# Optimization experiments

Measured on AMD Instinct MI355X. Metric: run time of the kernel, lower is better.

Reference implementation:

```python
import jax, jax.numpy as jnp
import numpy as np

NUM_CLASSES = 80
ANCHORS = np.array([[10,13],[16,30],[33,23],[30,61],[62,45],[59,119],[116,90],[156,198],[373,326]], np.float32)
MASK = [[0,1,2],[3,4,5],[6,7,8]]
STRIDES = [8, 16, 32]
MAX_OUT = 100      # max_output_size_per_class == max_total_size
IOU_THR = 0.45
SCORE_THR = 0.25
NMS_TOPK = 128     # per-class candidate pre-selection for greedy NMS (>= MAX_OUT)


def setup_inputs() -> dict:
    key = jax.random.key(0)
    k1, k2, k3 = jax.random.split(key, 3)
    B = 16
    C = 3 * (NUM_CLASSES + 5)  # 255
    return {
        'p3': jax.random.normal(k1, (B, 80, 80, C), jnp.float32),
        'p4': jax.random.normal(k2, (B, 40, 40, C), jnp.float32),
        'p5': jax.random.normal(k3, (B, 20, 20, C), jnp.float32),
    }


def _decode(logits, anchors, stride):
    # logits: [B,H,W,3*(nc+5)] -> boxes [B,H*W*3,4] (x1y1x2y2), obj [B,M], cls [B,M,nc]
    B, H, W, _ = logits.shape
    A = anchors.shape[0]
    x = logits.reshape(B, H, W, A, NUM_CLASSES + 5)
    xy = jax.nn.sigmoid(x[..., :2])
    wh_logit = x[..., 2:4]
    obj = jax.nn.sigmoid(x[..., 4])
    cls = jax.nn.sigmoid(x[..., 5:])
    gx, gy = jnp.meshgrid(jnp.arange(W, dtype=x.dtype), jnp.arange(H, dtype=x.dtype))
    grid = jnp.stack([gx, gy], axis=-1)[:, :, None, :]  # [H,W,1,2]
    ctr = (xy + grid) * stride
    wh = jnp.exp(wh_logit) * anchors  # [B,H,W,A,2]
    box = jnp.concatenate([ctr - wh / 2.0, ctr + wh / 2.0], axis=-1)
    return box.reshape(B, -1, 4), obj.reshape(B, -1), cls.reshape(B, -1, NUM_CLASSES)


def _pairwise_iou(b):
    # b: [K,4] x1y1x2y2 -> [K,K]
    area = (b[:, 2] - b[:, 0]) * (b[:, 3] - b[:, 1])
    lt = jnp.maximum(b[:, None, :2], b[None, :, :2])
    rb = jnp.minimum(b[:, None, 2:], b[None, :, 2:])
    wh = jnp.clip(rb - lt, 0.0)
    inter = wh[..., 0] * wh[..., 1]
    return inter / (area[:, None] + area[None, :] - inter + 1e-9)


def _nms_single(boxes, scores):
    # boxes [N,4], scores [N] for one (image, class): greedy NMS on top-K candidates
    s = jnp.where(scores > SCORE_THR, scores, -1.0)
    top_s, idx = jax.lax.top_k(s, NMS_TOPK)   # sorted descending
    b = boxes[idx]                            # [K,4]
    iou = _pairwise_iou(b)                    # [K,K]
    rng = jnp.arange(NMS_TOPK)

    def body(keep, i):
        active = keep[i] & (top_s[i] > 0.0)
        sup = active & (iou[i] > IOU_THR) & (rng > i)
        return keep & ~sup, None

    keep, _ = jax.lax.scan(body, jnp.ones(NMS_TOPK, bool), rng)
    valid = keep & (top_s > 0.0)
    ss = jnp.where(valid, top_s, -1.0)
    sel_s, sel_i = jax.lax.top_k(ss, MAX_OUT)
    return b[sel_i], sel_s                    # [M,4], [M]


def _per_image(boxes, scores_cn):
    # boxes [N,4] shared across classes (q=1), scores_cn [C,N]
    cb, cs = jax.vmap(_nms_single, in_axes=(None, 0))(boxes, scores_cn)  # [C,M,4],[C,M]
    C = cs.shape[0]
    cls_id = jnp.broadcast_to(jnp.arange(C, dtype=boxes.dtype)[:, None], cs.shape)
    fs, fi = jax.lax.top_k(cs.reshape(-1), MAX_OUT)
    fb = cb.reshape(-1, 4)[fi]
    fc = cls_id.reshape(-1)[fi]
    valid = fs > 0.0
    n_valid = jnp.sum(valid).astype(jnp.int32)
    return (jnp.where(valid[:, None], fb, 0.0),
            jnp.where(valid, fs, 0.0),
            jnp.where(valid, fc, 0.0),
            n_valid)


def _forward(p3, p4, p5):
    boxes, objs, clss = [], [], []
    for logits, m, stride in zip((p3, p4, p5), MASK, STRIDES):
        b, o, c = _decode(logits, jnp.asarray(ANCHORS[m]), float(stride))
        boxes.append(b); objs.append(o); clss.append(c)
    boxes = jnp.concatenate(boxes, axis=1)   # [B,N,4]
    obj = jnp.concatenate(objs, axis=1)      # [B,N]
    cls = jnp.concatenate(clss, axis=1)      # [B,N,C]
    scores = obj[..., None] * cls            # [B,N,C]
    return jax.vmap(_per_image)(boxes, scores.transpose(0, 2, 1))


def reference(p3, p4, p5):
    # returns (boxes [B,100,4], scores [B,100], classes [B,100], valid [B])
    return _forward(p3, p4, p5)
```

## Files before the change

### kernel.cpp

```cpp
#include <hip/hip_runtime.h>
#include <stdint.h>

#define NUM_CLASSES 80
#define N_ANCH 25200
#define B_IMG 16
#define NMS_TOPK_ 128
#define MAX_OUT_ 100
#define SCORE_THR_ 0.25f
#define IOU_THR_ 0.45f
#define NBINS 2048
#define CAP 2048
#define CAPB 512
#define CAPC 256
#define TILE_A 80

__constant__ float c_anch[9][2] = {
    {10.f, 13.f}, {16.f, 30.f}, {33.f, 23.f},
    {30.f, 61.f}, {62.f, 45.f}, {59.f, 119.f},
    {116.f, 90.f}, {156.f, 198.f}, {373.f, 326.f}};

__device__ __forceinline__ float sigmoidf_(float x) {
    return 1.0f / (1.0f + expf(-x));
}

__device__ __forceinline__ unsigned int score_bin(unsigned int bits) {
    unsigned int bin = (bits - 0x3E800000u) >> 13;
    if (bin >= NBINS) bin = NBINS - 1;
    return bin;
}


__global__ void __launch_bounds__(256) decode_scores_kernel(
    const float* __restrict__ p3, const float* __restrict__ p4,
    const float* __restrict__ p5, float* __restrict__ boxes,
    float* __restrict__ score_t) {
    int blk = blockIdx.x;
    int b = blk / 315;
    int tile = blk - b * 315;
    const float* p; int W, lvl, il0, base;
    if (tile < 240)      { p = p3; W = 80; lvl = 0; il0 = tile * TILE_A;         base = 0;     }
    else if (tile < 300) { p = p4; W = 40; lvl = 1; il0 = (tile - 240) * TILE_A; base = 19200; }
    else                 { p = p5; W = 20; lvl = 2; il0 = (tile - 300) * TILE_A; base = 24000; }
    float stride = (float)(8 << lvl);

    __shared__ float4 raw4[TILE_A * 85 / 4];
    __shared__ float obj_sh[TILE_A];
    float* raw = (float*)raw4;
    int tid = threadIdx.x;

    const float4* src4 = (const float4*)(p + (size_t)b * ((size_t)W * W * 255) +
                                         (size_t)il0 * 85);
    for (int k = tid; k < TILE_A * 85 / 4; k += 256) raw4[k] = src4[k];
    __syncthreads();

    if (tid < TILE_A) {
        int il = il0 + tid;
        int y = il / (W * 3);
        int t = il - y * (W * 3);
        int x = t / 3;
        int a = t - x * 3;
        const float* q = &raw[tid * 85];
        float cx = (sigmoidf_(q[0]) + (float)x) * stride;
        float cy = (sigmoidf_(q[1]) + (float)y) * stride;
        float bw = expf(q[2]) * c_anch[lvl * 3 + a][0];
        float bh = expf(q[3]) * c_anch[lvl * 3 + a][1];
        int gi = base + il;
        float* bo = boxes + ((size_t)b * N_ANCH + gi) * 4;
        bo[0] = cx - bw * 0.5f; bo[1] = cy - bh * 0.5f;
        bo[2] = cx + bw * 0.5f; bo[3] = cy + bh * 0.5f;
        obj_sh[tid] = sigmoidf_(q[4]);
    }
    __syncthreads();

    int gi0 = base + il0;
    for (int o = tid; o < NUM_CLASSES * (TILE_A / 4); o += 256) {
        int c = o / (TILE_A / 4);
        int q = o - c * (TILE_A / 4);
        int j = q * 4;
        float4 v;
        v.x = obj_sh[j + 0] * sigmoidf_(raw[(j + 0) * 85 + 5 + c]);
        v.y = obj_sh[j + 1] * sigmoidf_(raw[(j + 1) * 85 + 5 + c]);
        v.z = obj_sh[j + 2] * sigmoidf_(raw[(j + 2) * 85 + 5 + c]);
        v.w = obj_sh[j + 3] * sigmoidf_(raw[(j + 3) * 85 + 5 + c]);
        float4* dst = (float4*)(score_t + ((size_t)(b * NUM_CLASSES + c)) * N_ANCH + gi0);
        dst[q] = v;
    }
}

__global__ void __launch_bounds__(256) topk_nms_fast_kernel(
    const float* __restrict__ score_t, const float* __restrict__ boxes,
    float* __restrict__ cls_score, float* __restrict__ cls_box) {
    int b = blockIdx.x / NUM_CLASSES;
    int c = blockIdx.x % NUM_CLASSES;
    int tid = threadIdx.x;
    int lane = tid & 63;
    int wave = tid >> 6;
    const float4* sc4 = (const float4*)(score_t + (size_t)(b * NUM_CLASSES + c) * N_ANCH);

    __shared__ unsigned int hist[NBINS];
    __shared__ unsigned int segsum[256];
    __shared__ unsigned long long sel[CAPB];
    __shared__ float bx[NMS_TOPK_][5];
    __shared__ unsigned int s_cnt;
    __shared__ int s_cut;

    for (int k = tid; k < NBINS; k += 256) hist[k] = 0u;
    if (tid == 0) s_cnt = 0u;
    __syncthreads();

    for (int i = tid; i < N_ANCH / 4; i += 256) {
        float4 v = sc4[i];
        float vv[4] = {v.x, v.y, v.z, v.w};
#pragma unroll
        for (int k = 0; k < 4; ++k) {
            if (vv[k] > SCORE_THR_)
                atomicAdd(&hist[score_bin(__float_as_uint(vv[k]))], 1u);
        }
    }
    __syncthreads();

    unsigned int ss = 0;
    for (int k = 0; k < 8; ++k) ss += hist[tid * 8 + k];
    segsum[tid] = ss;
    __syncthreads();
    if (tid == 0) {
        unsigned int tot = 0; int cut = 0; int t = 255;
        for (; t >= 0; --t) {
            if (tot + segsum[t] >= NMS_TOPK_) break;
            tot += segsum[t];
        }
        if (t >= 0) {
            int j = 7;
            for (; j >= 0; --j) { tot += hist[t * 8 + j]; if (tot >= NMS_TOPK_) break; }
            if (j < 0) j = 0;
            cut = t * 8 + j;
        }
        s_cut = cut;
    }
    __syncthreads();
    unsigned int cutoff = (unsigned int)s_cut;

    for (int i = tid; i < N_ANCH / 4; i += 256) {
        float4 v = sc4[i];
        float vv[4] = {v.x, v.y, v.z, v.w};
#pragma unroll
        for (int k = 0; k < 4; ++k) {
            if (vv[k] > SCORE_THR_) {
                unsigned int bits = __float_as_uint(vv[k]);
                if (score_bin(bits) >= cutoff) {
                    unsigned int pos = atomicAdd(&s_cnt, 1u);
                    if (pos < CAPB) {
                        sel[pos] = ((unsigned long long)bits << 32) |
                                   (unsigned long long)(~(unsigned int)(i * 4 + k));
                    }
                }
            }
        }
    }
    __syncthreads();

    unsigned int M = s_cnt;
    if (M > CAPB) M = CAPB;
    unsigned int P2 = 1;
    while (P2 < M) P2 <<= 1;
    if (P2 < 2) P2 = 2;
    for (unsigned int k = M + tid; k < P2; k += 256) sel[k] = 0ull;
    __syncthreads();

    if (wave == 0) {
        for (unsigned int k = 2; k <= P2; k <<= 1) {
            for (unsigned int j = k >> 1; j > 0; j >>= 1) {
                for (unsigned int t = (unsigned int)lane; t < P2; t += 64) {
                    unsigned int ixj = t ^ j;
                    if (ixj > t) {
                        unsigned long long a0 = sel[t], b0 = sel[ixj];
                        bool desc = ((t & k) == 0);
                        if (desc ? (a0 < b0) : (a0 > b0)) { sel[t] = b0; sel[ixj] = a0; }
                    }
                }
                __threadfence_block();
            }
        }
    }
    __syncthreads();

    unsigned int K = M < NMS_TOPK_ ? M : NMS_TOPK_;
    if (tid < (int)K) {
        unsigned long long kk = sel[tid];
        unsigned int idx = ~((unsigned int)(kk & 0xFFFFFFFFull));
        const float* bp = boxes + ((size_t)b * N_ANCH + idx) * 4;
        bx[tid][0] = bp[0]; bx[tid][1] = bp[1];
        bx[tid][2] = bp[2]; bx[tid][3] = bp[3];
        bx[tid][4] = __uint_as_float((unsigned int)(kk >> 32));
    }
    __syncthreads();

    if (wave == 0) {
        bool k0 = (unsigned int)lane < K;
        bool k1 = (unsigned int)(64 + lane) < K;
        float x00 = 0, y00 = 0, x01 = 0, y01 = 0, a0 = 0, sv0 = 0;
        float x10 = 0, y10 = 0, x11 = 0, y11 = 0, a1 = 0, sv1 = 0;
        if (k0) {
            x00 = bx[lane][0]; y00 = bx[lane][1];
            x01 = bx[lane][2]; y01 = bx[lane][3]; sv0 = bx[lane][4];
            a0 = (x01 - x00) * (y01 - y00);
        }
        if (k1) {
            x10 = bx[64 + lane][0]; y10 = bx[64 + lane][1];
            x11 = bx[64 + lane][2]; y11 = bx[64 + lane][3]; sv1 = bx[64 + lane][4];
            a1 = (x11 - x10) * (y11 - y10);
        }
        unsigned long long km0 = __ballot(k0);
        unsigned long long km1 = __ballot(k1);
        for (unsigned int i = 0; i < K; ++i) {
            bool ki = ((((i < 64) ? km0 : km1) >> (i & 63)) & 1ull) != 0ull;
            if (ki) {
                float rx0 = bx[i][0], ry0 = bx[i][1], rx1 = bx[i][2], ry1 = bx[i][3];
                float ra = (rx1 - rx0) * (ry1 - ry0);
                if (k0 && (unsigned int)lane > i) {
                    float lx = fmaxf(rx0, x00), ly = fmaxf(ry0, y00);
                    float rx = fminf(rx1, x01), ry = fminf(ry1, y01);
                    float w = fmaxf(rx - lx, 0.f), h = fmaxf(ry - ly, 0.f);
                    float inter = w * h;
                    float iou = inter / (ra + a0 - inter + 1e-9f);
                    if (iou > IOU_THR_) k0 = false;
                }
                if (k1 && (unsigned int)(64 + lane) > i) {
                    float lx = fmaxf(rx0, x10), ly = fmaxf(ry0, y10);
                    float rx = fminf(rx1, x11), ry = fminf(ry1, y11);
                    float w = fmaxf(rx - lx, 0.f), h = fmaxf(ry - ly, 0.f);
                    float inter = w * h;
                    float iou = inter / (ra + a1 - inter + 1e-9f);
                    if (iou > IOU_THR_) k1 = false;
                }
                km0 = __ballot(k0);
                km1 = __ballot(k1);
            }
        }
        float* scd = cls_score + ((size_t)b * NUM_CLASSES + c) * MAX_OUT_;
        float* bod = cls_box + ((size_t)b * NUM_CLASSES + c) * (MAX_OUT_ * 4);
        int n0 = __popcll(km0);
        int n = n0 + __popcll(km1);
        if (k0) {
            int pos = __popcll(km0 & ((1ull << lane) - 1ull));
            if (pos < MAX_OUT_) {
                scd[pos] = sv0;
                bod[pos * 4 + 0] = x00; bod[pos * 4 + 1] = y00;
                bod[pos * 4 + 2] = x01; bod[pos * 4 + 3] = y01;
            }
        }
        if (k1) {
            int pos = n0 + __popcll(km1 & ((1ull << lane) - 1ull));
            if (pos < MAX_OUT_) {
                scd[pos] = sv1;
                bod[pos * 4 + 0] = x10; bod[pos * 4 + 1] = y10;
                bod[pos * 4 + 2] = x11; bod[pos * 4 + 3] = y11;
            }
        }
        int start = n < MAX_OUT_ ? n : MAX_OUT_;
        for (int p2 = start + lane; p2 < MAX_OUT_; p2 += 64) {
            scd[p2] = -1.0f;
            bod[p2 * 4 + 0] = 0.f; bod[p2 * 4 + 1] = 0.f;
            bod[p2 * 4 + 2] = 0.f; bod[p2 * 4 + 3] = 0.f;
        }
    }
}

__global__ void __launch_bounds__(256) final_fast_kernel(
    const float* __restrict__ cls_score, const float* __restrict__ cls_box,
    float* __restrict__ out) {
    int b = blockIdx.x;
    int tid = threadIdx.x;
    const int NC = NUM_CLASSES * MAX_OUT_;
    const float* sc = cls_score + (size_t)b * NC;

    __shared__ unsigned int hist[NBINS];
    __shared__ unsigned int segsum[256];
    __shared__ unsigned long long keys[CAPC];
    __shared__ unsigned int s_cnt, s_tot;
    __shared__ int s_cut;

    for (int k = tid; k < NBINS; k += 256) hist[k] = 0u;
    if (tid == 0) s_cnt = 0u;
    __syncthreads();

    for (int k = tid; k < NC; k += 256) {
        float s = sc[k];
        if (s > 0.0f) atomicAdd(&hist[score_bin(__float_as_uint(s))], 1u);
    }
    __syncthreads();

    unsigned int ss = 0;
    for (int k = 0; k < 8; ++k) ss += hist[tid * 8 + k];
    segsum[tid] = ss;
    __syncthreads();
    if (tid == 0) {
        unsigned int total = 0;
        for (int t = 0; t < 256; ++t) total += segsum[t];
        s_tot = total;
        unsigned int tot = 0; int cut = 0; int t = 255;
        for (; t >= 0; --t) {
            if (tot + segsum[t] >= MAX_OUT_) break;
            tot += segsum[t];
        }
        if (t >= 0) {
            int j = 7;
            for (; j >= 0; --j) { tot += hist[t * 8 + j]; if (tot >= MAX_OUT_) break; }
            if (j < 0) j = 0;
            cut = t * 8 + j;
        }
        s_cut = cut;
    }
    __syncthreads();
    unsigned int cutoff = (unsigned int)s_cut;

    for (int k = tid; k < NC; k += 256) {
        float s = sc[k];
        if (s > 0.0f && score_bin(__float_as_uint(s)) >= cutoff) {
            unsigned int pos = atomicAdd(&s_cnt, 1u);
            if (pos < CAPC) {
                keys[pos] = ((unsigned long long)__float_as_uint(s) << 32) |
                            (unsigned long long)(~(unsigned int)k);
            }
        }
    }
    __syncthreads();

    unsigned int M = s_cnt;
    if (M > CAPC) M = CAPC;
    unsigned int P2 = 1;
    while (P2 < M) P2 <<= 1;
    if (P2 < 2) P2 = 2;
    for (unsigned int k = M + tid; k < P2; k += 256) keys[k] = 0ull;
    __syncthreads();

    if (tid < 64) {
        for (unsigned int k = 2; k <= P2; k <<= 1) {
            for (unsigned int j = k >> 1; j > 0; j >>= 1) {
                for (unsigned int t = (unsigned int)tid; t < P2; t += 64) {
                    unsigned int ixj = t ^ j;
                    if (ixj > t) {
                        unsigned long long a0 = keys[t], b0 = keys[ixj];
                        bool desc = ((t & k) == 0);
                        if (desc ? (a0 < b0) : (a0 > b0)) { keys[t] = b0; keys[ixj] = a0; }
                    }
                }
                __threadfence_block();
            }
        }
    }
    __syncthreads();

    float* ob = out;
    float* os = out + B_IMG * MAX_OUT_ * 4;
    float* oc = os + B_IMG * MAX_OUT_;
    float* on = oc + B_IMG * MAX_OUT_;

    unsigned int K = M < MAX_OUT_ ? M : MAX_OUT_;
    if (tid < MAX_OUT_) {
        if ((unsigned int)tid < K) {
            unsigned long long kk = keys[tid];
            unsigned int flat = ~((unsigned int)(kk & 0xFFFFFFFFull));
            float sv = __uint_as_float((unsigned int)(kk >> 32));
            const float* bp = cls_box + ((size_t)b * NC + flat) * 4;
            os[b * MAX_OUT_ + tid] = sv;
            oc[b * MAX_OUT_ + tid] = (float)(flat / MAX_OUT_);
            ob[(b * MAX_OUT_ + tid) * 4 + 0] = bp[0];
            ob[(b * MAX_OUT_ + tid) * 4 + 1] = bp[1];
            ob[(b * MAX_OUT_ + tid) * 4 + 2] = bp[2];
            ob[(b * MAX_OUT_ + tid) * 4 + 3] = bp[3];
        } else {
            os[b * MAX_OUT_ + tid] = 0.0f;
            oc[b * MAX_OUT_ + tid] = 0.0f;
            ob[(b * MAX_OUT_ + tid) * 4 + 0] = 0.0f;
            ob[(b * MAX_OUT_ + tid) * 4 + 1] = 0.0f;
            ob[(b * MAX_OUT_ + tid) * 4 + 2] = 0.0f;
            ob[(b * MAX_OUT_ + tid) * 4 + 3] = 0.0f;
        }
    }
    if (tid == 0) {
        unsigned int nv = s_tot < MAX_OUT_ ? s_tot : MAX_OUT_;
        on[b] = (float)nv;
    }
}


__global__ void __launch_bounds__(256) decode_kernel(
    const float* __restrict__ p3, const float* __restrict__ p4,
    const float* __restrict__ p5, float* __restrict__ boxes,
    float* __restrict__ obj) {
    int gid = blockIdx.x * blockDim.x + threadIdx.x;
    if (gid >= B_IMG * N_ANCH) return;
    int b = gid / N_ANCH;
    int i = gid - b * N_ANCH;
    const float* p; int W, il, lvl; float stride;
    if (i < 19200)      { p = p3; W = 80; il = i;         lvl = 0; stride = 8.f;  }
    else if (i < 24000) { p = p4; W = 40; il = i - 19200; lvl = 1; stride = 16.f; }
    else                { p = p5; W = 20; il = i - 24000; lvl = 2; stride = 32.f; }
    int y = il / (W * 3);
    int t = il - y * W * 3;
    int x = t / 3;
    int a = t - x * 3;
    const float* q = p + ((((size_t)b * W + y) * W + x) * 255 + a * 85);
    float cx = (sigmoidf_(q[0]) + (float)x) * stride;
    float cy = (sigmoidf_(q[1]) + (float)y) * stride;
    float bw = expf(q[2]) * c_anch[lvl * 3 + a][0];
    float bh = expf(q[3]) * c_anch[lvl * 3 + a][1];
    float* bo = boxes + (size_t)gid * 4;
    bo[0] = cx - bw * 0.5f; bo[1] = cy - bh * 0.5f;
    bo[2] = cx + bw * 0.5f; bo[3] = cy + bh * 0.5f;
    obj[gid] = sigmoidf_(q[4]);
}

__device__ __forceinline__ float cand_score(
    const float* __restrict__ p3, const float* __restrict__ p4,
    const float* __restrict__ p5, const float* __restrict__ obj,
    int b, int c, int i) {
    const float* p; int W, il;
    if (i < 19200)      { p = p3; W = 80; il = i;         }
    else if (i < 24000) { p = p4; W = 40; il = i - 19200; }
    else                { p = p5; W = 20; il = i - 24000; }
    int y = il / (W * 3);
    int t = il - y * W * 3;
    int x = t / 3;
    int a = t - x * 3;
    float cl = p[(((size_t)b * W + y) * W + x) * 255 + a * 85 + 5 + c];
    return obj[b * N_ANCH + i] * sigmoidf_(cl);
}

__global__ void __launch_bounds__(256) topk_nms_kernel(
    const float* __restrict__ p3, const float* __restrict__ p4,
    const float* __restrict__ p5, const float* __restrict__ boxes,
    const float* __restrict__ obj, float* __restrict__ cls_score,
    float* __restrict__ cls_box) {
    int b = blockIdx.x / NUM_CLASSES;
    int c = blockIdx.x % NUM_CLASSES;
    int tid = threadIdx.x;

    __shared__ unsigned int hist[NBINS];
    __shared__ unsigned long long keys[CAP];
    __shared__ unsigned int s_cnt, s_cutoff;
    __shared__ float bx[NMS_TOPK_][5];
    __shared__ float bs[NMS_TOPK_];
    __shared__ int keep[NMS_TOPK_];

    for (int k = tid; k < NBINS; k += 256) hist[k] = 0u;
    if (tid == 0) s_cnt = 0u;
    __syncthreads();

    for (int i = tid; i < N_ANCH; i += 256) {
        float s = cand_score(p3, p4, p5, obj, b, c, i);
        if (s > SCORE_THR_) atomicAdd(&hist[score_bin(__float_as_uint(s))], 1u);
    }
    __syncthreads();

    if (tid == 0) {
        unsigned int total = 0;
        int cut = 0;
        for (int k = NBINS - 1; k >= 0; --k) {
            total += hist[k];
            if (total >= NMS_TOPK_) { cut = k; break; }
        }
        s_cutoff = (unsigned int)cut;
    }
    __syncthreads();
    unsigned int cutoff = s_cutoff;

    for (int i = tid; i < N_ANCH; i += 256) {
        float s = cand_score(p3, p4, p5, obj, b, c, i);
        if (s > SCORE_THR_) {
            unsigned int bits = __float_as_uint(s);
            if (score_bin(bits) >= cutoff) {
                unsigned int pos = atomicAdd(&s_cnt, 1u);
                if (pos < CAP) {
                    keys[pos] = ((unsigned long long)bits << 32) |
                                (unsigned long long)(~(unsigned int)i);
                }
            }
        }
    }
    __syncthreads();

    unsigned int M = s_cnt;
    if (M > CAP) M = CAP;
    unsigned int P2 = 1;
    while (P2 < M) P2 <<= 1;
    if (P2 < 2) P2 = 2;
    for (unsigned int k = M + tid; k < P2; k += 256) keys[k] = 0ull;
    __syncthreads();

    for (unsigned int k = 2; k <= P2; k <<= 1) {
        for (unsigned int j = k >> 1; j > 0; j >>= 1) {
            for (unsigned int t = tid; t < P2; t += 256) {
                unsigned int ixj = t ^ j;
                if (ixj > t) {
                    unsigned long long a0 = keys[t], b0 = keys[ixj];
                    bool desc = ((t & k) == 0);
                    if (desc ? (a0 < b0) : (a0 > b0)) { keys[t] = b0; keys[ixj] = a0; }
                }
            }
            __syncthreads();
        }
    }

    unsigned int K = M < NMS_TOPK_ ? M : NMS_TOPK_;
    if (tid < (int)K) {
        unsigned long long kk = keys[tid];
        unsigned int idx = ~((unsigned int)(kk & 0xFFFFFFFFull));
        const float* bp = boxes + ((size_t)b * N_ANCH + idx) * 4;
        bx[tid][0] = bp[0]; bx[tid][1] = bp[1];
        bx[tid][2] = bp[2]; bx[tid][3] = bp[3];
        bs[tid] = __uint_as_float((unsigned int)(kk >> 32));
        keep[tid] = 1;
    }
    __syncthreads();

    for (unsigned int i = 0; i < K; ++i) {
        if (keep[i]) {
            unsigned int t = (unsigned int)tid;
            if (t > i && t < K && keep[t]) {
                float ax0 = bx[i][0], ay0 = bx[i][1], ax1 = bx[i][2], ay1 = bx[i][3];
                float cx0 = bx[t][0], cy0 = bx[t][1], cx1 = bx[t][2], cy1 = bx[t][3];
                float areaA = (ax1 - ax0) * (ay1 - ay0);
                float areaB = (cx1 - cx0) * (cy1 - cy0);
                float lx = fmaxf(ax0, cx0), ly = fmaxf(ay0, cy0);
                float rx = fminf(ax1, cx1), ry = fminf(ay1, cy1);
                float w = rx - lx; if (w < 0.f) w = 0.f;
                float h = ry - ly; if (h < 0.f) h = 0.f;
                float inter = w * h;
                float iou = inter / (areaA + areaB - inter + 1e-9f);
                if (iou > IOU_THR_) keep[t] = 0;
            }
        }
        __syncthreads();
    }

    if (tid == 0) {
        float* scd = cls_score + ((size_t)b * NUM_CLASSES + c) * MAX_OUT_;
        float* bod = cls_box + ((size_t)b * NUM_CLASSES + c) * MAX_OUT_ * 4;
        int out_n = 0;
        for (unsigned int t2 = 0; t2 < K && out_n < MAX_OUT_; ++t2) {
            if (keep[t2]) {
                scd[out_n] = bs[t2];
                bod[out_n * 4 + 0] = bx[t2][0];
                bod[out_n * 4 + 1] = bx[t2][1];
                bod[out_n * 4 + 2] = bx[t2][2];
                bod[out_n * 4 + 3] = bx[t2][3];
                out_n++;
            }
        }
        for (; out_n < MAX_OUT_; ++out_n) {
            scd[out_n] = -1.0f;
            bod[out_n * 4 + 0] = 0.f; bod[out_n * 4 + 1] = 0.f;
            bod[out_n * 4 + 2] = 0.f; bod[out_n * 4 + 3] = 0.f;
        }
    }
}

extern "C" void kernel_launch(void* const* d_in, const int* in_sizes, int n_in,
                              void* d_out, int out_size, void* d_ws, size_t ws_size,
                              hipStream_t stream) {
    const float* p3 = (const float*)d_in[0];
    const float* p4 = (const float*)d_in[1];
    const float* p5 = (const float*)d_in[2];

    const size_t score_t_elems = (size_t)B_IMG * NUM_CLASSES * N_ANCH;
    const size_t boxes_elems   = (size_t)B_IMG * N_ANCH * 4;
    const size_t clsS_elems    = (size_t)B_IMG * NUM_CLASSES * MAX_OUT_;
    const size_t clsB_elems    = clsS_elems * 4;
    const size_t need_fast = (score_t_elems + boxes_elems + clsS_elems + clsB_elems) * sizeof(float);

    float* ws = (float*)d_ws;

    if (ws_size >= need_fast) {
        float* score_t   = ws;
        float* boxes     = score_t + score_t_elems;
        float* cls_score = boxes + boxes_elems;
        float* cls_box   = cls_score + clsS_elems;

        decode_scores_kernel<<<B_IMG * 315, 256, 0, stream>>>(p3, p4, p5, boxes, score_t);
        topk_nms_fast_kernel<<<B_IMG * NUM_CLASSES, 256, 0, stream>>>(
            score_t, boxes, cls_score, cls_box);
        final_fast_kernel<<<B_IMG, 256, 0, stream>>>(cls_score, cls_box, (float*)d_out);
    } else {
        float* boxes = ws;
        float* obj = boxes + boxes_elems;
        float* cls_score = obj + (size_t)B_IMG * N_ANCH;
        float* cls_box = cls_score + clsS_elems;

        int tot = B_IMG * N_ANCH;
        decode_kernel<<<(tot + 255) / 256, 256, 0, stream>>>(p3, p4, p5, boxes, obj);
        topk_nms_kernel<<<B_IMG * NUM_CLASSES, 256, 0, stream>>>(
            p3, p4, p5, boxes, obj, cls_score, cls_box);
        final_fast_kernel<<<B_IMG, 256, 0, stream>>>(cls_score, cls_box, (float*)d_out);
    }
}
```

Before: 333.3 us.

## Split top-K selection and NMS into separate kernels with single-wave NMS

Measured after the change: 324.5 us. 1.03x faster.

```diff
diff --git a/kernel.cpp b/kernel.cpp
--- a/kernel.cpp
+++ b/kernel.cpp
@@ -84,6 +84,198 @@
         v.w = obj_sh[j + 3] * sigmoidf_(raw[(j + 3) * 85 + 5 + c]);
         float4* dst = (float4*)(score_t + ((size_t)(b * NUM_CLASSES + c)) * N_ANCH + gi0);
         dst[q] = v;
+    }
+}
+
+__global__ void __launch_bounds__(256) select_topk_kernel(
+    const float* __restrict__ score_t,
+    unsigned long long* __restrict__ topsel) {
+    int tid = threadIdx.x;
+    const float4* sc4 = (const float4*)(score_t + (size_t)blockIdx.x * N_ANCH);
+
+    __shared__ unsigned int hist[NBINS];
+    __shared__ unsigned int segsum[256];
+    __shared__ unsigned long long sel[CAPB];
+    __shared__ unsigned int s_cnt;
+    __shared__ int s_cut;
+
+    for (int k = tid; k < NBINS; k += 256) hist[k] = 0u;
+    if (tid == 0) s_cnt = 0u;
+    __syncthreads();
+
+#pragma unroll 4
+    for (int i = tid; i < N_ANCH / 4; i += 256) {
+        float4 v = sc4[i];
+        float vv[4] = {v.x, v.y, v.z, v.w};
+#pragma unroll
+        for (int k = 0; k < 4; ++k) {
+            if (vv[k] > SCORE_THR_)
+                atomicAdd(&hist[score_bin(__float_as_uint(vv[k]))], 1u);
+        }
+    }
+    __syncthreads();
+
+    unsigned int ss = 0;
+    for (int k = 0; k < 8; ++k) ss += hist[tid * 8 + k];
+    segsum[tid] = ss;
+    __syncthreads();
+    if (tid == 0) {
+        unsigned int tot = 0; int cut = 0; int t = 255;
+        for (; t >= 0; --t) {
+            if (tot + segsum[t] >= NMS_TOPK_) break;
+            tot += segsum[t];
+        }
+        if (t >= 0) {
+            int j = 7;
+            for (; j >= 0; --j) { tot += hist[t * 8 + j]; if (tot >= NMS_TOPK_) break; }
+            if (j < 0) j = 0;
+            cut = t * 8 + j;
+        }
+        s_cut = cut;
+    }
+    __syncthreads();
+    unsigned int cutoff = (unsigned int)s_cut;
+
+#pragma unroll 2
+    for (int i = tid; i < N_ANCH / 4; i += 256) {
+        float4 v = sc4[i];
+        float vv[4] = {v.x, v.y, v.z, v.w};
+#pragma unroll
+        for (int k = 0; k < 4; ++k) {
+            if (vv[k] > SCORE_THR_) {
+                unsigned int bits = __float_as_uint(vv[k]);
+                if (score_bin(bits) >= cutoff) {
+                    unsigned int pos = atomicAdd(&s_cnt, 1u);
+                    if (pos < CAPB) {
+                        sel[pos] = ((unsigned long long)bits << 32) |
+                                   (unsigned long long)(~(unsigned int)(i * 4 + k));
+                    }
+                }
+            }
+        }
+    }
+    __syncthreads();
+
+    unsigned int M = s_cnt;
+    if (M > CAPB) M = CAPB;
+    unsigned int P2 = 1;
+    while (P2 < M) P2 <<= 1;
+    if (P2 < 2) P2 = 2;
+    for (unsigned int k = M + tid; k < P2; k += 256) sel[k] = 0ull;
+    __syncthreads();
+
+    for (unsigned int k = 2; k <= P2; k <<= 1) {
+        for (unsigned int j = k >> 1; j > 0; j >>= 1) {
+            for (unsigned int t = tid; t < (int)P2; t += 256) {
+                unsigned int ixj = (unsigned int)t ^ j;
+                if (ixj > (unsigned int)t) {
+                    unsigned long long a0 = sel[t], b0 = sel[ixj];
+                    bool desc = (((unsigned int)t & k) == 0);
+                    if (desc ? (a0 < b0) : (a0 > b0)) { sel[t] = b0; sel[ixj] = a0; }
+                }
+            }
+            __syncthreads();
+        }
+    }
+
+    unsigned long long* dst = topsel + (size_t)blockIdx.x * NMS_TOPK_;
+    if (tid < NMS_TOPK_) dst[tid] = ((unsigned int)tid < M) ? sel[tid] : 0ull;
+}
+
+__global__ void __launch_bounds__(64) nms_kernel(
+    const unsigned long long* __restrict__ topsel,
+    const float* __restrict__ boxes,
+    float* __restrict__ cls_score, float* __restrict__ cls_box) {
+    int bc = blockIdx.x;
+    int b = bc / NUM_CLASSES;
+    unsigned int lane = threadIdx.x;
+
+    __shared__ float bx[NMS_TOPK_][8];
+
+    const unsigned long long* src = topsel + (size_t)bc * NMS_TOPK_;
+    unsigned long long e0 = src[lane];
+    unsigned long long e1 = src[64 + lane];
+
+    bool k0 = (e0 != 0ull);
+    bool k1 = (e1 != 0ull);
+
+    float x00 = 0, y00 = 0, x01 = 0, y01 = 0, a0 = 0, sv0 = 0;
+    float x10 = 0, y10 = 0, x11 = 0, y11 = 0, a1 = 0, sv1 = 0;
+    if (k0) {
+        unsigned int idx = ~((unsigned int)(e0 & 0xFFFFFFFFull));
+        float4 bp = *(const float4*)(boxes + ((size_t)b * N_ANCH + idx) * 4);
+        x00 = bp.x; y00 = bp.y; x01 = bp.z; y01 = bp.w;
+        sv0 = __uint_as_float((unsigned int)(e0 >> 32));
+        a0 = (x01 - x00) * (y01 - y00);
+    }
+    if (k1) {
+        unsigned int idx = ~((unsigned int)(e1 & 0xFFFFFFFFull));
+        float4 bp = *(const float4*)(boxes + ((size_t)b * N_ANCH + idx) * 4);
+        x10 = bp.x; y10 = bp.y; x11 = bp.z; y11 = bp.w;
+        sv1 = __uint_as_float((unsigned int)(e1 >> 32));
+        a1 = (x11 - x10) * (y11 - y10);
+    }
+    {
+        float4 v0 = {x00, y00, x01, y01};
+        float4 v1 = {x10, y10, x11, y11};
+        *(float4*)&bx[lane][0] = v0;
+        *(float4*)&bx[64 + lane][0] = v1;
+    }
+    __syncthreads();
+
+    unsigned long long km0 = __ballot(k0);
+    unsigned long long km1 = __ballot(k1);
+    for (unsigned int i = 0; i < NMS_TOPK_; ++i) {
+        bool ki = ((((i < 64) ? km0 : km1) >> (i & 63)) & 1ull) != 0ull;
+        if (ki) {
+            float4 rb = *(const float4*)&bx[i][0];
+            float ra = (rb.z - rb.x) * (rb.w - rb.y);
+            if (k0 && lane > i) {
+                float lx = fmaxf(rb.x, x00), ly = fmaxf(rb.y, y00);
+                float rx = fminf(rb.z, x01), ry = fminf(rb.w, y01);
+                float w = fmaxf(rx - lx, 0.f), h = fmaxf(ry - ly, 0.f);
+                float inter = w * h;
+                float iou = inter / (ra + a0 - inter + 1e-9f);
+                if (iou > IOU_THR_) k0 = false;
+            }
+            if (k1 && (64 + lane) > i) {
+                float lx = fmaxf(rb.x, x10), ly = fmaxf(rb.y, y10);
+                float rx = fminf(rb.z, x11), ry = fminf(rb.w, y11);
+                float w = fmaxf(rx - lx, 0.f), h = fmaxf(ry - ly, 0.f);
+                float inter = w * h;
+                float iou = inter / (ra + a1 - inter + 1e-9f);
+                if (iou > IOU_THR_) k1 = false;
+            }
+            km0 = __ballot(k0);
+            km1 = __ballot(k1);
+        }
+    }
+
+    float* scd = cls_score + (size_t)bc * MAX_OUT_;
+    float* bod = cls_box + (size_t)bc * (MAX_OUT_ * 4);
+    int n0 = __popcll(km0);
+    int n = n0 + __popcll(km1);
+    if (k0) {
+        int pos = __popcll(km0 & ((1ull << lane) - 1ull));
+        if (pos < MAX_OUT_) {
+            scd[pos] = sv0;
+            bod[pos * 4 + 0] = x00; bod[pos * 4 + 1] = y00;
+            bod[pos * 4 + 2] = x01; bod[pos * 4 + 3] = y01;
+        }
+    }
+    if (k1) {
+        int pos = n0 + __popcll(km1 & ((1ull << lane) - 1ull));
+        if (pos < MAX_OUT_) {
+            scd[pos] = sv1;
+            bod[pos * 4 + 0] = x10; bod[pos * 4 + 1] = y10;
+            bod[pos * 4 + 2] = x11; bod[pos * 4 + 3] = y11;
+        }
+    }
+    int start = n < MAX_OUT_ ? n : MAX_OUT_;
+    for (int p2 = start + (int)lane; p2 < MAX_OUT_; p2 += 64) {
+        scd[p2] = -1.0f;
+        bod[p2 * 4 + 0] = 0.f; bod[p2 * 4 + 1] = 0.f;
+        bod[p2 * 4 + 2] = 0.f; bod[p2 * 4 + 3] = 0.f;
     }
 }
 
@@ -334,22 +526,19 @@
     for (unsigned int k = M + tid; k < P2; k += 256) keys[k] = 0ull;
     __syncthreads();
 
-    if (tid < 64) {
-        for (unsigned int k = 2; k <= P2; k <<= 1) {
-            for (unsigned int j = k >> 1; j > 0; j >>= 1) {
-                for (unsigned int t = (unsigned int)tid; t < P2; t += 64) {
-                    unsigned int ixj = t ^ j;
-                    if (ixj > t) {
-                        unsigned long long a0 = keys[t], b0 = keys[ixj];
-                        bool desc = ((t & k) == 0);
-                        if (desc ? (a0 < b0) : (a0 > b0)) { keys[t] = b0; keys[ixj] = a0; }
-                    }
+    for (unsigned int k = 2; k <= P2; k <<= 1) {
+        for (unsigned int j = k >> 1; j > 0; j >>= 1) {
+            for (unsigned int t = (unsigned int)tid; t < P2; t += 256) {
+                unsigned int ixj = t ^ j;
+                if (ixj > t) {
+                    unsigned long long a0 = keys[t], b0 = keys[ixj];
+                    bool desc = ((t & k) == 0);
+                    if (desc ? (a0 < b0) : (a0 > b0)) { keys[t] = b0; keys[ixj] = a0; }
                 }
-                __threadfence_block();
-            }
-        }
-    }
-    __syncthreads();
+            }
+            __syncthreads();
+        }
+    }
 
     float* ob = out;
     float* os = out + B_IMG * MAX_OUT_ * 4;
@@ -568,11 +757,25 @@
     const size_t boxes_elems   = (size_t)B_IMG * N_ANCH * 4;
     const size_t clsS_elems    = (size_t)B_IMG * NUM_CLASSES * MAX_OUT_;
     const size_t clsB_elems    = clsS_elems * 4;
+    const size_t topsel_bytes  = (size_t)B_IMG * NUM_CLASSES * NMS_TOPK_ *
+                                 sizeof(unsigned long long);
     const size_t need_fast = (score_t_elems + boxes_elems + clsS_elems + clsB_elems) * sizeof(float);
+    const size_t need_full = need_fast + topsel_bytes;
 
     float* ws = (float*)d_ws;
 
-    if (ws_size >= need_fast) {
+    if (ws_size >= need_full) {
+        float* score_t   = ws;
+        float* boxes     = score_t + score_t_elems;
+        float* cls_score = boxes + boxes_elems;
+        float* cls_box   = cls_score + clsS_elems;
+        unsigned long long* topsel = (unsigned long long*)(cls_box + clsB_elems);
+
+        decode_scores_kernel<<<B_IMG * 315, 256, 0, stream>>>(p3, p4, p5, boxes, score_t);
+        select_topk_kernel<<<B_IMG * NUM_CLASSES, 256, 0, stream>>>(score_t, topsel);
+        nms_kernel<<<B_IMG * NUM_CLASSES, 64, 0, stream>>>(topsel, boxes, cls_score, cls_box);
+        final_fast_kernel<<<B_IMG, 256, 0, stream>>>(cls_score, cls_box, (float*)d_out);
+    } else if (ws_size >= need_fast) {
         float* score_t   = ws;
         float* boxes     = score_t + score_t_elems;
         float* cls_score = boxes + boxes_elems;
```

## Store class scores as truncated 16-bit, recompute exact scores for candidates, split NMS

Applied to the files above, without the earlier changes.

Result: faster. 312.1 us (-6.4%).

```diff
diff --git a/kernel.cpp b/kernel.cpp
--- a/kernel.cpp
+++ b/kernel.cpp
@@ -10,9 +10,9 @@
 #define IOU_THR_ 0.45f
 #define NBINS 2048
 #define CAP 2048
-#define CAPB 512
+#define CAPB 1024
 #define CAPC 256
-#define TILE_A 80
+#define U16_THR 0x3E80u
 
 __constant__ float c_anch[9][2] = {
     {10.f, 13.f}, {16.f, 30.f}, {33.f, 23.f},
@@ -30,30 +30,31 @@
 }
 
 
-__global__ void __launch_bounds__(256) decode_scores_kernel(
+__global__ void __launch_bounds__(256) decode_scores_u16_kernel(
     const float* __restrict__ p3, const float* __restrict__ p4,
     const float* __restrict__ p5, float* __restrict__ boxes,
-    float* __restrict__ score_t) {
+    unsigned short* __restrict__ score_u) {
     int blk = blockIdx.x;
-    int b = blk / 315;
-    int tile = blk - b * 315;
-    const float* p; int W, lvl, il0, base;
-    if (tile < 240)      { p = p3; W = 80; lvl = 0; il0 = tile * TILE_A;         base = 0;     }
-    else if (tile < 300) { p = p4; W = 40; lvl = 1; il0 = (tile - 240) * TILE_A; base = 19200; }
-    else                 { p = p5; W = 20; lvl = 2; il0 = (tile - 300) * TILE_A; base = 24000; }
+    int b = blk / 405;
+    int tile = blk - b * 405;
+    const float* p; int W, lvl, il0, base, ta;
+    if (tile < 300)      { p = p3; W = 80; lvl = 0; ta = 64; il0 = tile * 64;         base = 0;     }
+    else if (tile < 375) { p = p4; W = 40; lvl = 1; ta = 64; il0 = (tile - 300) * 64; base = 19200; }
+    else                 { p = p5; W = 20; lvl = 2; ta = 40; il0 = (tile - 375) * 40; base = 24000; }
     float stride = (float)(8 << lvl);
 
-    __shared__ float4 raw4[TILE_A * 85 / 4];
-    __shared__ float obj_sh[TILE_A];
+    __shared__ float4 raw4[64 * 85 / 4];
+    __shared__ float obj_sh[64];
     float* raw = (float*)raw4;
     int tid = threadIdx.x;
 
     const float4* src4 = (const float4*)(p + (size_t)b * ((size_t)W * W * 255) +
                                          (size_t)il0 * 85);
-    for (int k = tid; k < TILE_A * 85 / 4; k += 256) raw4[k] = src4[k];
-    __syncthreads();
-
-    if (tid < TILE_A) {
+    int n4 = ta * 85 / 4;
+    for (int k = tid; k < n4; k += 256) raw4[k] = src4[k];
+    __syncthreads();
+
+    if (tid < ta) {
         int il = il0 + tid;
         int y = il / (W * 3);
         int t = il - y * (W * 3);
@@ -73,86 +74,83 @@
     __syncthreads();
 
     int gi0 = base + il0;
-    for (int o = tid; o < NUM_CLASSES * (TILE_A / 4); o += 256) {
-        int c = o / (TILE_A / 4);
-        int q = o - c * (TILE_A / 4);
-        int j = q * 4;
-        float4 v;
-        v.x = obj_sh[j + 0] * sigmoidf_(raw[(j + 0) * 85 + 5 + c]);
-        v.y = obj_sh[j + 1] * sigmoidf_(raw[(j + 1) * 85 + 5 + c]);
-        v.z = obj_sh[j + 2] * sigmoidf_(raw[(j + 2) * 85 + 5 + c]);
-        v.w = obj_sh[j + 3] * sigmoidf_(raw[(j + 3) * 85 + 5 + c]);
-        float4* dst = (float4*)(score_t + ((size_t)(b * NUM_CLASSES + c)) * N_ANCH + gi0);
-        dst[q] = v;
-    }
-}
-
-__global__ void __launch_bounds__(256) topk_nms_fast_kernel(
-    const float* __restrict__ score_t, const float* __restrict__ boxes,
-    float* __restrict__ cls_score, float* __restrict__ cls_box) {
-    int b = blockIdx.x / NUM_CLASSES;
-    int c = blockIdx.x % NUM_CLASSES;
+    int gpc = ta >> 3;
+    int ng = NUM_CLASSES * gpc;
+    for (int o = tid; o < ng; o += 256) {
+        int c, g;
+        if (gpc == 8) { c = o >> 3; g = o & 7; }
+        else          { c = o / 5;  g = o - c * 5; }
+        int j = g * 8;
+        unsigned int w[4];
+#pragma unroll
+        for (int k = 0; k < 4; ++k) {
+            float s0 = obj_sh[j + 2 * k]     * sigmoidf_(raw[(j + 2 * k) * 85 + 5 + c]);
+            float s1 = obj_sh[j + 2 * k + 1] * sigmoidf_(raw[(j + 2 * k + 1) * 85 + 5 + c]);
+            w[k] = (__float_as_uint(s0) >> 16) | (__float_as_uint(s1) & 0xFFFF0000u);
+        }
+        uint4 v = {w[0], w[1], w[2], w[3]};
+        *(uint4*)(score_u + ((size_t)(b * NUM_CLASSES + c)) * N_ANCH + gi0 + j) = v;
+    }
+}
+
+__global__ void __launch_bounds__(256) select_topk_u16_kernel(
+    const unsigned short* __restrict__ score_u,
+    const float* __restrict__ p3, const float* __restrict__ p4,
+    const float* __restrict__ p5,
+    unsigned long long* __restrict__ topsel) {
+    int bc = blockIdx.x;
+    int b = bc / NUM_CLASSES;
+    int c = bc - b * NUM_CLASSES;
     int tid = threadIdx.x;
-    int lane = tid & 63;
-    int wave = tid >> 6;
-    const float4* sc4 = (const float4*)(score_t + (size_t)(b * NUM_CLASSES + c) * N_ANCH);
-
-    __shared__ unsigned int hist[NBINS];
-    __shared__ unsigned int segsum[256];
+    const uint4* sc = (const uint4*)(score_u + (size_t)bc * N_ANCH);
+
+    __shared__ unsigned int hist[256];
     __shared__ unsigned long long sel[CAPB];
-    __shared__ float bx[NMS_TOPK_][5];
     __shared__ unsigned int s_cnt;
     __shared__ int s_cut;
 
-    for (int k = tid; k < NBINS; k += 256) hist[k] = 0u;
+    hist[tid] = 0u;
     if (tid == 0) s_cnt = 0u;
     __syncthreads();
 
-    for (int i = tid; i < N_ANCH / 4; i += 256) {
-        float4 v = sc4[i];
-        float vv[4] = {v.x, v.y, v.z, v.w};
+    for (int i = tid; i < N_ANCH / 8; i += 256) {
+        uint4 v = sc[i];
+        unsigned int ww[4] = {v.x, v.y, v.z, v.w};
 #pragma unroll
-        for (int k = 0; k < 4; ++k) {
-            if (vv[k] > SCORE_THR_)
-                atomicAdd(&hist[score_bin(__float_as_uint(vv[k]))], 1u);
-        }
-    }
-    __syncthreads();
-
-    unsigned int ss = 0;
-    for (int k = 0; k < 8; ++k) ss += hist[tid * 8 + k];
-    segsum[tid] = ss;
-    __syncthreads();
+        for (int k = 0; k < 8; ++k) {
+            unsigned int h = (ww[k >> 1] >> ((k & 1) * 16)) & 0xFFFFu;
+            if (h >= U16_THR) {
+                unsigned int bin = h - U16_THR;
+                if (bin > 255u) bin = 255u;
+                atomicAdd(&hist[bin], 1u);
+            }
+        }
+    }
+    __syncthreads();
+
     if (tid == 0) {
-        unsigned int tot = 0; int cut = 0; int t = 255;
-        for (; t >= 0; --t) {
-            if (tot + segsum[t] >= NMS_TOPK_) break;
-            tot += segsum[t];
-        }
-        if (t >= 0) {
-            int j = 7;
-            for (; j >= 0; --j) { tot += hist[t * 8 + j]; if (tot >= NMS_TOPK_) break; }
-            if (j < 0) j = 0;
-            cut = t * 8 + j;
+        unsigned int tot = 0; int cut = 0;
+        for (int t = 255; t >= 0; --t) {
+            tot += hist[t];
+            if (tot >= NMS_TOPK_) { cut = t; break; }
         }
         s_cut = cut;
     }
     __syncthreads();
     unsigned int cutoff = (unsigned int)s_cut;
 
-    for (int i = tid; i < N_ANCH / 4; i += 256) {
-        float4 v = sc4[i];
-        float vv[4] = {v.x, v.y, v.z, v.w};
+    for (int i = tid; i < N_ANCH / 8; i += 256) {
+        uint4 v = sc[i];
+        unsigned int ww[4] = {v.x, v.y, v.z, v.w};
 #pragma unroll
-        for (int k = 0; k < 4; ++k) {
-            if (vv[k] > SCORE_THR_) {
-                unsigned int bits = __float_as_uint(vv[k]);
-                if (score_bin(bits) >= cutoff) {
+        for (int k = 0; k < 8; ++k) {
+            unsigned int h = (ww[k >> 1] >> ((k & 1) * 16)) & 0xFFFFu;
+            if (h >= U16_THR) {
+                unsigned int bin = h - U16_THR;
+                if (bin > 255u) bin = 255u;
+                if (bin >= cutoff) {
                     unsigned int pos = atomicAdd(&s_cnt, 1u);
-                    if (pos < CAPB) {
-                        sel[pos] = ((unsigned long long)bits << 32) |
-                                   (unsigned long long)(~(unsigned int)(i * 4 + k));
-                    }
+                    if (pos < CAPB) sel[pos] = (unsigned long long)(i * 8 + k);
                 }
             }
         }
@@ -161,108 +159,139 @@
 
     unsigned int M = s_cnt;
     if (M > CAPB) M = CAPB;
+
+    for (unsigned int t = tid; t < M; t += 256) {
+        unsigned int idx = (unsigned int)sel[t];
+        const float* q;
+        if (idx < 19200u)      q = p3 + (size_t)b * 1632000 + (size_t)idx * 85;
+        else if (idx < 24000u) q = p4 + (size_t)b * 408000 + (size_t)(idx - 19200u) * 85;
+        else                   q = p5 + (size_t)b * 102000 + (size_t)(idx - 24000u) * 85;
+        float s = sigmoidf_(q[4]) * sigmoidf_(q[5 + c]);
+        sel[t] = (s > SCORE_THR_)
+                     ? (((unsigned long long)__float_as_uint(s) << 32) |
+                        (unsigned long long)(~idx))
+                     : 0ull;
+    }
+    __syncthreads();
+
     unsigned int P2 = 1;
     while (P2 < M) P2 <<= 1;
     if (P2 < 2) P2 = 2;
     for (unsigned int k = M + tid; k < P2; k += 256) sel[k] = 0ull;
     __syncthreads();
 
-    if (wave == 0) {
-        for (unsigned int k = 2; k <= P2; k <<= 1) {
-            for (unsigned int j = k >> 1; j > 0; j >>= 1) {
-                for (unsigned int t = (unsigned int)lane; t < P2; t += 64) {
-                    unsigned int ixj = t ^ j;
-                    if (ixj > t) {
-                        unsigned long long a0 = sel[t], b0 = sel[ixj];
-                        bool desc = ((t & k) == 0);
-                        if (desc ? (a0 < b0) : (a0 > b0)) { sel[t] = b0; sel[ixj] = a0; }
-                    }
+    for (unsigned int k = 2; k <= P2; k <<= 1) {
+        for (unsigned int j = k >> 1; j > 0; j >>= 1) {
+            for (unsigned int t = tid; t < (int)P2; t += 256) {
+                unsigned int ixj = (unsigned int)t ^ j;
+                if (ixj > (unsigned int)t) {
+                    unsigned long long a0 = sel[t], b0 = sel[ixj];
+                    bool desc = (((unsigned int)t & k) == 0);
+                    if (desc ? (a0 < b0) : (a0 > b0)) { sel[t] = b0; sel[ixj] = a0; }
                 }
-                __threadfence_block();
-            }
-        }
-    }
-    __syncthreads();
-
-    unsigned int K = M < NMS_TOPK_ ? M : NMS_TOPK_;
-    if (tid < (int)K) {
-        unsigned long long kk = sel[tid];
-        unsigned int idx = ~((unsigned int)(kk & 0xFFFFFFFFull));
-        const float* bp = boxes + ((size_t)b * N_ANCH + idx) * 4;
-        bx[tid][0] = bp[0]; bx[tid][1] = bp[1];
-        bx[tid][2] = bp[2]; bx[tid][3] = bp[3];
-        bx[tid][4] = __uint_as_float((unsigned int)(kk >> 32));
-    }
-    __syncthreads();
-
-    if (wave == 0) {
-        bool k0 = (unsigned int)lane < K;
-        bool k1 = (unsigned int)(64 + lane) < K;
-        float x00 = 0, y00 = 0, x01 = 0, y01 = 0, a0 = 0, sv0 = 0;
-        float x10 = 0, y10 = 0, x11 = 0, y11 = 0, a1 = 0, sv1 = 0;
-        if (k0) {
-            x00 = bx[lane][0]; y00 = bx[lane][1];
-            x01 = bx[lane][2]; y01 = bx[lane][3]; sv0 = bx[lane][4];
-            a0 = (x01 - x00) * (y01 - y00);
-        }
-        if (k1) {
-            x10 = bx[64 + lane][0]; y10 = bx[64 + lane][1];
-            x11 = bx[64 + lane][2]; y11 = bx[64 + lane][3]; sv1 = bx[64 + lane][4];
-            a1 = (x11 - x10) * (y11 - y10);
-        }
-        unsigned long long km0 = __ballot(k0);
-        unsigned long long km1 = __ballot(k1);
-        for (unsigned int i = 0; i < K; ++i) {
-            bool ki = ((((i < 64) ? km0 : km1) >> (i & 63)) & 1ull) != 0ull;
-            if (ki) {
-                float rx0 = bx[i][0], ry0 = bx[i][1], rx1 = bx[i][2], ry1 = bx[i][3];
-                float ra = (rx1 - rx0) * (ry1 - ry0);
-                if (k0 && (unsigned int)lane > i) {
-                    float lx = fmaxf(rx0, x00), ly = fmaxf(ry0, y00);
-                    float rx = fminf(rx1, x01), ry = fminf(ry1, y01);
-                    float w = fmaxf(rx - lx, 0.f), h = fmaxf(ry - ly, 0.f);
-                    float inter = w * h;
-                    float iou = inter / (ra + a0 - inter + 1e-9f);
-                    if (iou > IOU_THR_) k0 = false;
-                }
-                if (k1 && (unsigned int)(64 + lane) > i) {
-                    float lx = fmaxf(rx0, x10), ly = fmaxf(ry0, y10);
-                    float rx = fminf(rx1, x11), ry = fminf(ry1, y11);
-                    float w = fmaxf(rx - lx, 0.f), h = fmaxf(ry - ly, 0.f);
-                    float inter = w * h;
-                    float iou = inter / (ra + a1 - inter + 1e-9f);
-                    if (iou > IOU_THR_) k1 = false;
-                }
-                km0 = __ballot(k0);
-                km1 = __ballot(k1);
-            }
-        }
-        float* scd = cls_score + ((size_t)b * NUM_CLASSES + c) * MAX_OUT_;
-        float* bod = cls_box + ((size_t)b * NUM_CLASSES + c) * (MAX_OUT_ * 4);
-        int n0 = __popcll(km0);
-        int n = n0 + __popcll(km1);
-        if (k0) {
-            int pos = __popcll(km0 & ((1ull << lane) - 1ull));
-            if (pos < MAX_OUT_) {
-                scd[pos] = sv0;
-                bod[pos * 4 + 0] = x00; bod[pos * 4 + 1] = y00;
-                bod[pos * 4 + 2] = x01; bod[pos * 4 + 3] = y01;
-            }
-        }
-        if (k1) {
-            int pos = n0 + __popcll(km1 & ((1ull << lane) - 1ull));
-            if (pos < MAX_OUT_) {
-                scd[pos] = sv1;
-                bod[pos * 4 + 0] = x10; bod[pos * 4 + 1] = y10;
-                bod[pos * 4 + 2] = x11; bod[pos * 4 + 3] = y11;
-            }
-        }
-        int start = n < MAX_OUT_ ? n : MAX_OUT_;
-        for (int p2 = start + lane; p2 < MAX_OUT_; p2 += 64) {
-            scd[p2] = -1.0f;
-            bod[p2 * 4 + 0] = 0.f; bod[p2 * 4 + 1] = 0.f;
-            bod[p2 * 4 + 2] = 0.f; bod[p2 * 4 + 3] = 0.f;
-        }
+            }
+            __syncthreads();
+        }
+    }
+
+    unsigned long long* dst = topsel + (size_t)bc * NMS_TOPK_;
+    if (tid < NMS_TOPK_) dst[tid] = ((unsigned int)tid < M) ? sel[tid] : 0ull;
+}
+
+__global__ void __launch_bounds__(64) nms_kernel(
+    const unsigned long long* __restrict__ topsel,
+    const float* __restrict__ boxes,
+    float* __restrict__ cls_score, float* __restrict__ cls_box) {
+    int bc = blockIdx.x;
+    int b = bc / NUM_CLASSES;
+    unsigned int lane = threadIdx.x;
+
+    __shared__ float bx[NMS_TOPK_][8];
+
+    const unsigned long long* src = topsel + (size_t)bc * NMS_TOPK_;
+    unsigned long long e0 = src[lane];
+    unsigned long long e1 = src[64 + lane];
+
+    bool k0 = (e0 != 0ull);
+    bool k1 = (e1 != 0ull);
+
+    float x00 = 0, y00 = 0, x01 = 0, y01 = 0, a0 = 0, sv0 = 0;
+    float x10 = 0, y10 = 0, x11 = 0, y11 = 0, a1 = 0, sv1 = 0;
+    if (k0) {
+        unsigned int idx = ~((unsigned int)(e0 & 0xFFFFFFFFull));
+        float4 bp = *(const float4*)(boxes + ((size_t)b * N_ANCH + idx) * 4);
+        x00 = bp.x; y00 = bp.y; x01 = bp.z; y01 = bp.w;
+        sv0 = __uint_as_float((unsigned int)(e0 >> 32));
+        a0 = (x01 - x00) * (y01 - y00);
+    }
+    if (k1) {
+        unsigned int idx = ~((unsigned int)(e1 & 0xFFFFFFFFull));
+        float4 bp = *(const float4*)(boxes + ((size_t)b * N_ANCH + idx) * 4);
+        x10 = bp.x; y10 = bp.y; x11 = bp.z; y11 = bp.w;
+        sv1 = __uint_as_float((unsigned int)(e1 >> 32));
+        a1 = (x11 - x10) * (y11 - y10);
+    }
+    {
+        float4 v0 = {x00, y00, x01, y01};
+        float4 v1 = {x10, y10, x11, y11};
+        *(float4*)&bx[lane][0] = v0;
+        *(float4*)&bx[64 + lane][0] = v1;
+    }
+    __syncthreads();
+
+    unsigned long long km0 = __ballot(k0);
+    unsigned long long km1 = __ballot(k1);
+    for (unsigned int i = 0; i < NMS_TOPK_; ++i) {
+        bool ki = ((((i < 64) ? km0 : km1) >> (i & 63)) & 1ull) != 0ull;
+        if (ki) {
+            float4 rb = *(const float4*)&bx[i][0];
+            float ra = (rb.z - rb.x) * (rb.w - rb.y);
+            if (k0 && lane > i) {
+                float lx = fmaxf(rb.x, x00), ly = fmaxf(rb.y, y00);
+                float rx = fminf(rb.z, x01), ry = fminf(rb.w, y01);
+                float w = fmaxf(rx - lx, 0.f), h = fmaxf(ry - ly, 0.f);
+                float inter = w * h;
+                float iou = inter / (ra + a0 - inter + 1e-9f);
+                if (iou > IOU_THR_) k0 = false;
+            }
+            if (k1 && (64 + lane) > i) {
+                float lx = fmaxf(rb.x, x10), ly = fmaxf(rb.y, y10);
+                float rx = fminf(rb.z, x11), ry = fminf(rb.w, y11);
+                float w = fmaxf(rx - lx, 0.f), h = fmaxf(ry - ly, 0.f);
+                float inter = w * h;
+                float iou = inter / (ra + a1 - inter + 1e-9f);
+                if (iou > IOU_THR_) k1 = false;
+            }
+            km0 = __ballot(k0);
+            km1 = __ballot(k1);
+        }
+    }
+
+    float* scd = cls_score + (size_t)bc * MAX_OUT_;
+    float* bod = cls_box + (size_t)bc * (MAX_OUT_ * 4);
+    int n0 = __popcll(km0);
+    int n = n0 + __popcll(km1);
+    if (k0) {
+        int pos = __popcll(km0 & ((1ull << lane) - 1ull));
+        if (pos < MAX_OUT_) {
+            scd[pos] = sv0;
+            bod[pos * 4 + 0] = x00; bod[pos * 4 + 1] = y00;
+            bod[pos * 4 + 2] = x01; bod[pos * 4 + 3] = y01;
+        }
+    }
+    if (k1) {
+        int pos = n0 + __popcll(km1 & ((1ull << lane) - 1ull));
+        if (pos < MAX_OUT_) {
+            scd[pos] = sv1;
+            bod[pos * 4 + 0] = x10; bod[pos * 4 + 1] = y10;
+            bod[pos * 4 + 2] = x11; bod[pos * 4 + 3] = y11;
+        }
+    }
+    int start = n < MAX_OUT_ ? n : MAX_OUT_;
+    for (int p2 = start + (int)lane; p2 < MAX_OUT_; p2 += 64) {
+        scd[p2] = -1.0f;
+        bod[p2 * 4 + 0] = 0.f; bod[p2 * 4 + 1] = 0.f;
+        bod[p2 * 4 + 2] = 0.f; bod[p2 * 4 + 3] = 0.f;
     }
 }
 
@@ -334,22 +363,19 @@
     for (unsigned int k = M + tid; k < P2; k += 256) keys[k] = 0ull;
     __syncthreads();
 
-    if (tid < 64) {
-        for (unsigned int k = 2; k <= P2; k <<= 1) {
-            for (unsigned int j = k >> 1; j > 0; j >>= 1) {
-                for (unsigned int t = (unsigned int)tid; t < P2; t += 64) {
-                    unsigned int ixj = t ^ j;
-                    if (ixj > t) {
-                        unsigned long long a0 = keys[t], b0 = keys[ixj];
-                        bool desc = ((t & k) == 0);
-                        if (desc ? (a0 < b0) : (a0 > b0)) { keys[t] = b0; keys[ixj] = a0; }
-                    }
+    for (unsigned int k = 2; k <= P2; k <<= 1) {
+        for (unsigned int j = k >> 1; j > 0; j >>= 1) {
+            for (unsigned int t = (unsigned int)tid; t < P2; t += 256) {
+                unsigned int ixj = t ^ j;
+                if (ixj > t) {
+                    unsigned long long a0 = keys[t], b0 = keys[ixj];
+                    bool desc = ((t & k) == 0);
+                    if (desc ? (a0 < b0) : (a0 > b0)) { keys[t] = b0; keys[ixj] = a0; }
                 }
-                __threadfence_block();
-            }
-        }
-    }
-    __syncthreads();
+            }
+            __syncthreads();
+        }
+    }
 
     float* ob = out;
     float* os = out + B_IMG * MAX_OUT_ * 4;
@@ -564,29 +590,36 @@
     const float* p4 = (const float*)d_in[1];
     const float* p5 = (const float*)d_in[2];
 
-    const size_t score_t_elems = (size_t)B_IMG * NUM_CLASSES * N_ANCH;
-    const size_t boxes_elems   = (size_t)B_IMG * N_ANCH * 4;
-    const size_t clsS_elems    = (size_t)B_IMG * NUM_CLASSES * MAX_OUT_;
-    const size_t clsB_elems    = clsS_elems * 4;
-    const size_t need_fast = (score_t_elems + boxes_elems + clsS_elems + clsB_elems) * sizeof(float);
-
-    float* ws = (float*)d_ws;
-
-    if (ws_size >= need_fast) {
-        float* score_t   = ws;
-        float* boxes     = score_t + score_t_elems;
-        float* cls_score = boxes + boxes_elems;
-        float* cls_box   = cls_score + clsS_elems;
-
-        decode_scores_kernel<<<B_IMG * 315, 256, 0, stream>>>(p3, p4, p5, boxes, score_t);
-        topk_nms_fast_kernel<<<B_IMG * NUM_CLASSES, 256, 0, stream>>>(
-            score_t, boxes, cls_score, cls_box);
+    const size_t boxesB  = (size_t)B_IMG * N_ANCH * 4 * sizeof(float);
+    const size_t clsSB   = (size_t)B_IMG * NUM_CLASSES * MAX_OUT_ * sizeof(float);
+    const size_t clsBB   = clsSB * 4;
+    const size_t topselB = (size_t)B_IMG * NUM_CLASSES * NMS_TOPK_ * 8;
+    const size_t scoreUB = (size_t)B_IMG * NUM_CLASSES * N_ANCH * 2;
+    const size_t need_new = boxesB + clsSB + clsBB + topselB + scoreUB;
+
+    char* base = (char*)d_ws;
+
+    if (ws_size >= need_new) {
+        float* boxes     = (float*)base;
+        float* cls_score = (float*)(base + boxesB);
+        float* cls_box   = (float*)(base + boxesB + clsSB);
+        unsigned long long* topsel =
+            (unsigned long long*)(base + boxesB + clsSB + clsBB);
+        unsigned short* score_u =
+            (unsigned short*)(base + boxesB + clsSB + clsBB + topselB);
+
+        decode_scores_u16_kernel<<<B_IMG * 405, 256, 0, stream>>>(
+            p3, p4, p5, boxes, score_u);
+        select_topk_u16_kernel<<<B_IMG * NUM_CLASSES, 256, 0, stream>>>(
+            score_u, p3, p4, p5, topsel);
+        nms_kernel<<<B_IMG * NUM_CLASSES, 64, 0, stream>>>(
+            topsel, boxes, cls_score, cls_box);
         final_fast_kernel<<<B_IMG, 256, 0, stream>>>(cls_score, cls_box, (float*)d_out);
     } else {
-        float* boxes = ws;
-        float* obj = boxes + boxes_elems;
+        float* boxes = (float*)base;
+        float* obj = boxes + (size_t)B_IMG * N_ANCH * 4;
         float* cls_score = obj + (size_t)B_IMG * N_ANCH;
-        float* cls_box = cls_score + clsS_elems;
+        float* cls_box = cls_score + (size_t)B_IMG * NUM_CLASSES * MAX_OUT_;
 
         int tot = B_IMG * N_ANCH;
         decode_kernel<<<(tot + 255) / 256, 256, 0, stream>>>(p3, p4, p5, boxes, obj);
```
